# Performance work log

Hardware: AMD Instinct MI355X
Metric: run time of the kernel (lower is better)

## Reference

```python
import jax, jax.numpy as jnp
import numpy as np


def setup_inputs() -> dict:
    key = jax.random.key(0)
    k1, k2 = jax.random.split(key)
    # x: (B, C, D, H, W); w: (out_ch, C * 2*2*2)
    x = jax.random.normal(k1, (4, 64, 33, 33, 33), dtype=jnp.float32)
    w = jax.random.normal(k2, (128, 64 * 8), dtype=jnp.float32) * 0.05
    return {"x": x, "w": w}


def reference(x, w):
    # unfoldNd(kernel=2, stride=1, pad=0) + einsum('ij,kjm->kim', w, patches)
    # is exactly a valid 3D cross-correlation with a 2x2x2 kernel.
    B, C, D, H, W = x.shape
    O = w.shape[0]
    kern = w.reshape(O, C, 2, 2, 2)  # unfold flattening order: (C, kd, kh, kw)
    y = jax.lax.conv_general_dilated(
        x, kern,
        window_strides=(1, 1, 1),
        padding='VALID',
        dimension_numbers=('NCDHW', 'OIDHW', 'NCDHW'),
    )  # (B, O, D-1, H-1, W-1)
    return (y + 1.0) ** 2
```

## Files before the change

kernel.cpp:

```cpp
#include <hip/hip_runtime.h>

typedef __bf16 bf16x8 __attribute__((ext_vector_type(8)));
typedef float f32x4 __attribute__((ext_vector_type(4)));
typedef unsigned short u16;
typedef unsigned int u32;
typedef u32 u32x4 __attribute__((ext_vector_type(4)));
typedef u16 u16x8 __attribute__((ext_vector_type(8)));

__device__ __forceinline__ u16 f32_to_bf16_rne(float f) {
    union { float f; unsigned u; } cv; cv.f = f;
    unsigned u = cv.u;
    return (u16)((u + 0x7FFFu + ((u >> 16) & 1u)) >> 16);
}

__device__ __forceinline__ u32 cvt_pk_bf16(float lo, float hi) {
    u32 r;
    asm("v_cvt_pk_bf16_f32 %0, %1, %2" : "=v"(r) : "v"(lo), "v"(hi));
    return r;
}

__global__ void repack_w_kernel(const float* __restrict__ w, u16* __restrict__ w3) {
    int e = blockIdx.x * 256 + threadIdx.x;
    int j    = e & 7;
    int g    = (e >> 3) & 3;
    int o    = (e >> 5) & 127;
    int cb   = (e >> 12) & 1;
    int koff = (e >> 13) & 7;
    int c = (cb << 5) + (g << 3) + j;
    w3[e] = f32_to_bf16_rne(w[(o << 9) + (c << 3) + koff]);
}

#define XS_ROW 72

__global__ __launch_bounds__(256, 4) void conv_mfma_kernel(
    const float* __restrict__ x, const u16* __restrict__ w3, float* __restrict__ out) {

    __shared__ __align__(16) u16 xs[6 * 33 * XS_ROW];

    const int tid = threadIdx.x;
    const int bid = blockIdx.x;
    const int hy0 = (bid & 15) << 1;
    const int dz  = (bid >> 4) & 31;
    const int b   = bid >> 9;

    const float* xb = x + (size_t)b * 64 * 35937;
    for (int i = tid; i < 1584; i += 256) {
        int w   = i % 33;
        int t   = i / 33;
        int q   = t & 7;
        int kh3 = t >> 3;
        int kd  = kh3 >= 3 ? 1 : 0;
        int kh  = kh3 - kd * 3;
        const float* p = xb + (size_t)(q << 3) * 35937 + (dz + kd) * 1089 + (hy0 + kh) * 33 + w;
        float f0 = p[0],          f1 = p[35937],     f2 = p[2 * 35937], f3 = p[3 * 35937];
        float f4 = p[4 * 35937],  f5 = p[5 * 35937], f6 = p[6 * 35937], f7 = p[7 * 35937];
        u32x4 v;
        v[0] = cvt_pk_bf16(f0, f1);
        v[1] = cvt_pk_bf16(f2, f3);
        v[2] = cvt_pk_bf16(f4, f5);
        v[3] = cvt_pk_bf16(f6, f7);
        *reinterpret_cast<u32x4*>(&xs[(kh3 * 33 + w) * XS_ROW + (q << 3)]) = v;
    }
    __syncthreads();

    const int lane = tid & 63;
    const int ln   = lane & 15;
    const int g    = lane >> 4;
    const int n0w  = (tid >> 6) << 5;

    f32x4 acc[2][4];
#pragma unroll
    for (int nf = 0; nf < 2; ++nf)
#pragma unroll
        for (int mf = 0; mf < 4; ++mf)
            acc[nf][mf] = (f32x4){0.f, 0.f, 0.f, 0.f};

#pragma unroll
    for (int cb = 0; cb < 2; ++cb) {
        const int cbase = (cb << 5) + (g << 3);
#pragma unroll
        for (int kd = 0; kd < 2; ++kd) {
            bf16x8 wf[2][4];
#pragma unroll
            for (int nf = 0; nf < 2; ++nf)
#pragma unroll
                for (int kk = 0; kk < 4; ++kk) {
                    const int koff = (kd << 2) + kk;
                    const u16* p = w3 + (size_t)((((koff << 1) + cb) << 7)
                                   + n0w + (nf << 4) + ln) * 32 + (g << 3);
                    wf[nf][kk] = __builtin_bit_cast(bf16x8, *reinterpret_cast<const u16x8*>(p));
                }
#pragma unroll
            for (int kw = 0; kw < 2; ++kw) {
                bf16x8 xf[3][2];
#pragma unroll
                for (int hh = 0; hh < 3; ++hh)
#pragma unroll
                    for (int wh = 0; wh < 2; ++wh) {
                        const int row = (kd * 3 + hh) * 33 + (wh << 4) + ln + kw;
                        xf[hh][wh] = __builtin_bit_cast(bf16x8,
                            *reinterpret_cast<const u16x8*>(&xs[row * XS_ROW + cbase]));
                    }
#pragma unroll
                for (int kh = 0; kh < 2; ++kh)
#pragma unroll
                    for (int nf = 0; nf < 2; ++nf)
#pragma unroll
                        for (int mf = 0; mf < 4; ++mf)
                            acc[nf][mf] = __builtin_amdgcn_mfma_f32_16x16x32_bf16(
                                wf[nf][(kh << 1) + kw], xf[(mf >> 1) + kh][mf & 1],
                                acc[nf][mf], 0, 0, 0);
            }
        }
    }

    float* ob = out + ((size_t)b * 128) * 32768 + (dz << 10) + (hy0 << 5);
#pragma unroll
    for (int nf = 0; nf < 2; ++nf)
#pragma unroll
        for (int mf = 0; mf < 4; ++mf) {
            const int wx   = ((mf & 1) << 4) + ln;
            const int hrow = mf >> 1;
            float* o2 = ob + (hrow << 5) + wx;
#pragma unroll
            for (int r = 0; r < 4; ++r) {
                const int n = n0w + (nf << 4) + (g << 2) + r;
                float v = acc[nf][mf][r] + 1.0f;
                o2[(size_t)n << 15] = v * v;
            }
        }
}

extern "C" void kernel_launch(void* const* d_in, const int* in_sizes, int n_in,
                              void* d_out, int out_size, void* d_ws, size_t ws_size,
                              hipStream_t stream) {
    const float* x = (const float*)d_in[0];
    const float* w = (const float*)d_in[1];
    float* out = (float*)d_out;
    u16* w3 = (u16*)d_ws;

    repack_w_kernel<<<256, 256, 0, stream>>>(w, w3);
    conv_mfma_kernel<<<2048, 256, 0, stream>>>(x, w3, out);
}
```

Before: 49.01 us.

## Pre-transpose x to channel-last bf16 and stage slabs via global_load_lds

Adds a pre-pass kernel that converts x to bf16 in a channel-blocked row layout, with a separate buffer holding the w=32 edge column. The conv kernel then loads its six input slabs straight into LDS with 16-byte global_load_lds, replacing the strided fp32 gathers and in-kernel conversion. The aim is to cut redundant strided global reads and conversion work, since each x row is reused by many blocks. The cost is an extra kernel launch and a full write and re-read of a bf16 copy of x through the workspace. The old path is kept as a fallback when the workspace is too small.

```diff
diff --git a/kernel.cpp b/kernel.cpp
--- a/kernel.cpp
+++ b/kernel.cpp
@@ -6,6 +6,11 @@
 typedef unsigned int u32;
 typedef u32 u32x4 __attribute__((ext_vector_type(4)));
 typedef u16 u16x8 __attribute__((ext_vector_type(8)));
+
+#define AS1 __attribute__((address_space(1)))
+#define AS3 __attribute__((address_space(3)))
+#define GLL16(gp, lp) __builtin_amdgcn_global_load_lds((const AS1 void*)(gp), (AS3 void*)(lp), 16, 0, 0)
+#define GLL4(gp, lp)  __builtin_amdgcn_global_load_lds((const AS1 void*)(gp), (AS3 void*)(lp), 4, 0, 0)
 
 __device__ __forceinline__ u16 f32_to_bf16_rne(float f) {
     union { float f; unsigned u; } cv; cv.f = f;
@@ -30,9 +35,151 @@
     w3[e] = f32_to_bf16_rne(w[(o << 9) + (c << 3) + koff]);
 }
 
+__global__ __launch_bounds__(256) void transpose_x_kernel(
+    const float* __restrict__ x, u16* __restrict__ xT, u16* __restrict__ x32) {
+
+    __shared__ float t[64][34];
+    const int bid = blockIdx.x;
+    const int h = bid % 33;
+    const int dq = bid / 33;
+    const int d = dq % 33;
+    const int b = dq / 33;
+    const float* xp = x + (size_t)b * 2299968 + d * 1089 + h * 33;
+
+    const int tid = threadIdx.x;
+    const int wv  = tid & 31;
+    const int c0  = tid >> 5;
+#pragma unroll
+    for (int i = 0; i < 8; ++i) {
+        int c = c0 + (i << 3);
+        t[c][wv] = xp[(size_t)c * 35937 + wv];
+    }
+    if (tid < 64) t[tid][32] = xp[(size_t)tid * 35937 + 32];
+    __syncthreads();
+
+    const int cc = tid >> 5;
+    u32x4 v;
+    v[0] = cvt_pk_bf16(t[cc * 8 + 0][wv], t[cc * 8 + 1][wv]);
+    v[1] = cvt_pk_bf16(t[cc * 8 + 2][wv], t[cc * 8 + 3][wv]);
+    v[2] = cvt_pk_bf16(t[cc * 8 + 4][wv], t[cc * 8 + 5][wv]);
+    v[3] = cvt_pk_bf16(t[cc * 8 + 6][wv], t[cc * 8 + 7][wv]);
+    *reinterpret_cast<u32x4*>(&xT[(size_t)bid * 2048 + cc * 256 + wv * 8]) = v;
+
+    if (tid < 8) {
+        u32x4 m;
+        m[0] = cvt_pk_bf16(t[tid * 8 + 0][32], t[tid * 8 + 1][32]);
+        m[1] = cvt_pk_bf16(t[tid * 8 + 2][32], t[tid * 8 + 3][32]);
+        m[2] = cvt_pk_bf16(t[tid * 8 + 4][32], t[tid * 8 + 5][32]);
+        m[3] = cvt_pk_bf16(t[tid * 8 + 6][32], t[tid * 8 + 7][32]);
+        *reinterpret_cast<u32x4*>(&x32[(size_t)bid * 64 + tid * 8]) = m;
+    }
+}
+
+__global__ __launch_bounds__(256, 4) void conv_mfma_kernel(
+    const u16* __restrict__ xT, const u16* __restrict__ x32,
+    const u16* __restrict__ w3, float* __restrict__ out) {
+
+    __shared__ __align__(16) u16 xs[12672];
+
+    const int tid = threadIdx.x;
+    const int bid = blockIdx.x;
+    const int hy0 = (bid & 15) << 1;
+    const int dz  = (bid >> 4) & 31;
+    const int b   = bid >> 9;
+
+    char* ldsb = (char*)xs;
+    const int wave_off = (tid >> 6) << 10;
+#pragma unroll
+    for (int s = 0; s < 6; ++s) {
+        const int kd = (s >= 3) ? 1 : 0;
+        const int kh = s - kd * 3;
+        const size_t gslab = (size_t)(b * 1089 + (dz + kd) * 33 + (hy0 + kh));
+        const char* src = (const char*)xT + (gslab << 12) + (tid << 4);
+        GLL16(src, ldsb + (s << 12) + wave_off + ((tid & 63) << 4));
+    }
+    if (tid < 192) {
+        const int kd = tid / 96;
+        const int r  = (tid << 2) - kd * 384;
+        const char* src = (const char*)x32
+            + ((size_t)(b * 1089 + (dz + kd) * 33 + hy0) << 7) + r;
+        GLL4(src, ldsb + 24576 + ((tid >> 6) << 8) + ((tid & 63) << 2));
+    }
+    asm volatile("s_waitcnt vmcnt(0)" ::: "memory");
+    __syncthreads();
+
+    const int lane = tid & 63;
+    const int ln   = lane & 15;
+    const int g    = lane >> 4;
+    const int n0w  = (tid >> 6) << 5;
+
+    f32x4 acc[2][4];
+#pragma unroll
+    for (int nf = 0; nf < 2; ++nf)
+#pragma unroll
+        for (int mf = 0; mf < 4; ++mf)
+            acc[nf][mf] = (f32x4){0.f, 0.f, 0.f, 0.f};
+
+#pragma unroll
+    for (int cb = 0; cb < 2; ++cb) {
+        const int cc = (cb << 2) + g;
+#pragma unroll
+        for (int kd = 0; kd < 2; ++kd) {
+            bf16x8 wf[2][4];
+#pragma unroll
+            for (int nf = 0; nf < 2; ++nf)
+#pragma unroll
+                for (int kk = 0; kk < 4; ++kk) {
+                    const int koff = (kd << 2) + kk;
+                    const u16* p = w3 + (size_t)((((koff << 1) + cb) << 7)
+                                   + n0w + (nf << 4) + ln) * 32 + (g << 3);
+                    wf[nf][kk] = __builtin_bit_cast(bf16x8, *reinterpret_cast<const u16x8*>(p));
+                }
+#pragma unroll
+            for (int kw = 0; kw < 2; ++kw) {
+                bf16x8 xf[3][2];
+#pragma unroll
+                for (int hh = 0; hh < 3; ++hh)
+#pragma unroll
+                    for (int wh = 0; wh < 2; ++wh) {
+                        const int row = (wh << 4) + ln + kw;
+                        const u16* p = (row < 32)
+                            ? &xs[(((kd * 3 + hh) << 11)) + (cc << 8) + (row << 3)]
+                            : &xs[12288 + kd * 192 + hh * 64 + (cc << 3)];
+                        xf[hh][wh] = __builtin_bit_cast(bf16x8,
+                            *reinterpret_cast<const u16x8*>(p));
+                    }
+#pragma unroll
+                for (int kh = 0; kh < 2; ++kh)
+#pragma unroll
+                    for (int nf = 0; nf < 2; ++nf)
+#pragma unroll
+                        for (int mf = 0; mf < 4; ++mf)
+                            acc[nf][mf] = __builtin_amdgcn_mfma_f32_16x16x32_bf16(
+                                wf[nf][(kh << 1) + kw], xf[(mf >> 1) + kh][mf & 1],
+                                acc[nf][mf], 0, 0, 0);
+            }
+        }
+    }
+
+    float* ob = out + ((size_t)b * 128) * 32768 + (dz << 10) + (hy0 << 5);
+#pragma unroll
+    for (int nf = 0; nf < 2; ++nf)
+#pragma unroll
+        for (int mf = 0; mf < 4; ++mf) {
+            const int wx   = ((mf & 1) << 4) + ln;
+            const int hrow = mf >> 1;
+            float* o2 = ob + (hrow << 5) + wx;
+#pragma unroll
+            for (int r = 0; r < 4; ++r) {
+                const int n = n0w + (nf << 4) + (g << 2) + r;
+                float v = acc[nf][mf][r] + 1.0f;
+                o2[(size_t)n << 15] = v * v;
+            }
+        }
+}
+
 #define XS_ROW 72
-
-__global__ __launch_bounds__(256, 4) void conv_mfma_kernel(
+__global__ __launch_bounds__(256, 4) void conv_mfma_fallback(
     const float* __restrict__ x, const u16* __restrict__ w3, float* __restrict__ out) {
 
     __shared__ __align__(16) u16 xs[6 * 33 * XS_ROW];
@@ -52,13 +199,11 @@
         int kd  = kh3 >= 3 ? 1 : 0;
         int kh  = kh3 - kd * 3;
         const float* p = xb + (size_t)(q << 3) * 35937 + (dz + kd) * 1089 + (hy0 + kh) * 33 + w;
-        float f0 = p[0],          f1 = p[35937],     f2 = p[2 * 35937], f3 = p[3 * 35937];
-        float f4 = p[4 * 35937],  f5 = p[5 * 35937], f6 = p[6 * 35937], f7 = p[7 * 35937];
         u32x4 v;
-        v[0] = cvt_pk_bf16(f0, f1);
-        v[1] = cvt_pk_bf16(f2, f3);
-        v[2] = cvt_pk_bf16(f4, f5);
-        v[3] = cvt_pk_bf16(f6, f7);
+        v[0] = cvt_pk_bf16(p[0], p[35937]);
+        v[1] = cvt_pk_bf16(p[2 * 35937], p[3 * 35937]);
+        v[2] = cvt_pk_bf16(p[4 * 35937], p[5 * 35937]);
+        v[3] = cvt_pk_bf16(p[6 * 35937], p[7 * 35937]);
         *reinterpret_cast<u32x4*>(&xs[(kh3 * 33 + w) * XS_ROW + (q << 3)]) = v;
     }
     __syncthreads();
@@ -137,8 +282,21 @@
     const float* x = (const float*)d_in[0];
     const float* w = (const float*)d_in[1];
     float* out = (float*)d_out;
+
+    const size_t W3_BYTES  = 131072;
+    const size_t XT_BYTES  = (size_t)4356 * 4096;
+    const size_t X32_BYTES = (size_t)4356 * 128;
+    const size_t NEED = W3_BYTES + XT_BYTES + X32_BYTES;
+
     u16* w3 = (u16*)d_ws;
-
     repack_w_kernel<<<256, 256, 0, stream>>>(w, w3);
-    conv_mfma_kernel<<<2048, 256, 0, stream>>>(x, w3, out);
-}
+
+    if (ws_size >= NEED) {
+        u16* xT  = (u16*)((char*)d_ws + W3_BYTES);
+        u16* x32 = (u16*)((char*)d_ws + W3_BYTES + XT_BYTES);
+        transpose_x_kernel<<<4356, 256, 0, stream>>>(x, xT, x32);
+        conv_mfma_kernel<<<2048, 256, 0, stream>>>(xT, x32, w3, out);
+    } else {
+        conv_mfma_fallback<<<2048, 256, 0, stream>>>(x, w3, out);
+    }
+}
```

Measured after the change: 51.95 us. 6.0% more time.
